# Performance work log

Hardware: AMD Instinct MI355X
Metric: run time of the kernel (lower is better)

The kernel has to match this reference:

```python
import jax, jax.numpy as jnp
from jax import lax
import numpy as np

NSTART, NOPEN, NHID, NCLOSE, NLAYERS, KSZ, N = 40, 128, 256, 3, 40, 9, 1024
H_STEP = 0.1
PAD = (KSZ - 1) // 2  # 4 -> same-length conv
EPS = 1e-5


def conv1(x, K):
    # x: (1, Cin, N), K: (Cout, Cin, k); cross-correlation like torch F.conv1d
    return lax.conv_general_dilated(x, K, (1,), [(PAD, PAD)],
                                    dimension_numbers=('NCH', 'OIH', 'NCH'))


def conv1T(x, K):
    # torch F.conv_transpose1d(x, K, padding=PAD) == conv1d with swapped-channel,
    # flipped kernel and padding k-1-PAD (= PAD here since k=9, PAD=4)
    Kt = jnp.flip(jnp.swapaxes(K, 0, 1), -1)
    return lax.conv_general_dilated(x, Kt, (1,), [(PAD, PAD)],
                                    dimension_numbers=('NCH', 'OIH', 'NCH'))


def instance_norm(x):
    # x: (1, C, N); normalize per channel over spatial dim, biased var, no affine
    m = jnp.mean(x, axis=-1, keepdims=True)
    v = jnp.var(x, axis=-1, keepdims=True)
    return (x - m) * lax.rsqrt(v + EPS)


def get_graph_lap(Z):
    # Z: (C, N). Normalized Gaussian-affinity graph Laplacian.
    sq = jnp.sum(Z * Z, axis=0)  # (N,)
    D2 = jnp.maximum(sq[:, None] + sq[None, :] - 2.0 * (Z.T @ Z), 0.0)
    sigma = jnp.mean(D2) + 1e-12
    Wg = jnp.exp(-D2 / sigma)
    deg = jnp.sum(Wg, axis=1)
    Dh = lax.rsqrt(deg)
    L = Dh[:, None] * (jnp.diag(deg) - Wg) * Dh[None, :]
    return L, deg


def double_sym_layer(Z, Wi, Bi, L):
    # Z: (nopen, N), Wi: (2, nhid, nopen, 9), Bi: (2, nopen, 1), L: (N, N)
    A0 = instance_norm(conv1((Z + Bi[0])[None], Wi[0]))
    A1 = instance_norm((conv1((Z + Bi[1])[None], Wi[1])[0] @ L)[None])
    A0 = jax.nn.relu(A0)
    A1 = jax.nn.relu(A1)
    A0 = conv1T(A0, Wi[0])[0]
    A1 = conv1T(A1, Wi[1])[0] @ L.T
    return A0 + A1  # (nopen, N)


def setup_inputs() -> dict:
    key = jax.random.key(0)
    k1, k2, k3, k4, k5 = jax.random.split(key, 5)
    Z = jax.random.normal(k1, (NSTART, N), dtype=jnp.float32)
    stdv_o = 0.001 * NOPEN / NSTART
    Kopen = jax.random.uniform(k2, (NOPEN, NSTART), minval=-stdv_o, maxval=stdv_o, dtype=jnp.float32)
    stdv_c = 0.001 * NCLOSE / NOPEN
    Kclose = jax.random.uniform(k3, (NCLOSE, NOPEN), minval=-stdv_c, maxval=stdv_c, dtype=jnp.float32)
    W = jax.random.uniform(k4, (NLAYERS, 2, NHID, NOPEN, KSZ), minval=-1e-4, maxval=1e-4, dtype=jnp.float32)
    Bias = jax.random.uniform(k5, (NLAYERS, 2, NOPEN, 1), dtype=jnp.float32) * 1e-4
    return {"Z": Z, "Kopen": Kopen, "Kclose": Kclose, "W": W, "Bias": Bias}


def reference(Z, Kopen, Kclose, W, Bias):
    h = H_STEP
    Zc = Kopen @ Z          # (nopen, N)
    Zold = Zc
    L, _ = get_graph_lap(Zc)
    for i in range(NLAYERS):
        if i % 10 == 0:
            L, _ = get_graph_lap(Zc)
        Ai = double_sym_layer(Zc, W[i], Bias[i], L)
        Zc, Zold = 2.0 * Zc - Zold - (h * h) * Ai, Zc  # leapfrog step
    return (Kclose @ Zc, Kclose @ Zold)
```

## Files before the change

kernel.cpp:

```cpp
#include <hip/hip_runtime.h>

#define NN 1024
#define NOPEN 128
#define NHID 256
#define NSTART 40
#define NCLOSE 3
#define NLAYERS 40
#define KSZ 9

static constexpr float H2 = 0.01f;
static constexpr float IN_EPS = 1e-5f;

using floatx4 = __attribute__((ext_vector_type(4))) float;
using bfrag = __attribute__((ext_vector_type(8))) short;

__device__ __forceinline__ ushort f2bf(float f) {
    union { float f; unsigned u; } v; v.f = f;
    unsigned r = v.u + 0x7fffu + ((v.u >> 16) & 1u);
    return (ushort)(r >> 16);
}

__device__ __forceinline__ void prepw_piece(const float* __restrict__ W, ushort* __restrict__ Wf1,
                                            ushort* __restrict__ Wf2, int lb, int lsrc, int tid) {
    if (lb < 72) {
        int z = lb / 36, rem = lb % 36;
        int t = rem >> 2, q = rem & 3;
        const float* Wz = W + (size_t)(lsrc * 2 + z) * (NHID * NOPEN * KSZ);
        ushort* dst = Wf1 + (((size_t)(z * 9 + t) * 64 + q * 16) << 9);
#pragma unroll
        for (int r = 0; r < 32; ++r) {
            int ei = r * 256 + tid;
            int g = q * 4 + (ei >> 11);
            int kc = (ei >> 9) & 3;
            int lm = (ei >> 3) & 15, lq = (ei >> 7) & 3;
            int e = ei & 7;
            int co = g * 16 + lm, ci = kc * 32 + lq * 8 + e;
            dst[ei] = f2bf(Wz[co * (NOPEN * KSZ) + ci * KSZ + t]);
        }
    } else {
        int p2 = lb - 72;
        int z = p2 / 36, rem = p2 % 36;
        int t = rem >> 2, q = rem & 3;
        const float* Wz = W + (size_t)(lsrc * 2 + z) * (NHID * NOPEN * KSZ);
        ushort* dst = Wf2 + (((size_t)(z * 9 + t) * 64 + q * 16) << 9);
#pragma unroll
        for (int r = 0; r < 32; ++r) {
            int ei = r * 256 + tid;
            int fb = q * 16 + (ei >> 9);
            int g = fb >> 3, j = fb & 7;
            int lm = (ei >> 3) & 15, lq = (ei >> 7) & 3;
            int e = ei & 7;
            int ci = g * 16 + lm, co = j * 32 + lq * 8 + e;
            dst[ei] = f2bf(Wz[co * (NOPEN * KSZ) + ci * KSZ + t]);
        }
    }
}

__global__ __launch_bounds__(256) void k_open(const float* __restrict__ Kopen, const float* __restrict__ Z,
                       float* __restrict__ Zc, float* __restrict__ Zold,
                       const float* __restrict__ Bias0, ushort* __restrict__ Zct,
                       ushort* __restrict__ At0, ushort* __restrict__ At1,
                       const float* __restrict__ W, ushort* __restrict__ Wf1,
                       ushort* __restrict__ Wf2, float* __restrict__ sig, float* __restrict__ A1) {
    const int v = blockIdx.x, tid = threadIdx.x;
    if (v < 512) {
        int o = v >> 2, n = (v & 3) * 256 + tid;
        float acc = 0.f;
#pragma unroll
        for (int s = 0; s < NSTART; ++s)
            acc = fmaf(Kopen[o * NSTART + s], Z[s * NN + n], acc);
        Zc[o * NN + n] = acc;
        Zold[o * NN + n] = acc;
#pragma unroll
        for (int z = 0; z < 2; ++z)
            Zct[z * (1032 * 128) + (n + 4) * 128 + o] = f2bf(acc + Bias0[z * NOPEN + o]);
    } else if (v < 656) {
        prepw_piece(W, Wf1, Wf2, v - 512, 0, tid);
    } else if (v == 656) {
        if (tid == 0) sig[0] = 0.f;
        for (int idx = tid; idx < 1024; idx += 256) {
            int z = idx >> 9, rr = idx & 511;
            ushort* Zz = Zct + z * (1032 * 128);
            Zz[rr] = 0; Zz[1028 * 128 + rr] = 0;
        }
        for (int idx = tid; idx < 2048; idx += 256) {
            int a = idx >> 10, rr = idx & 1023;
            ushort* A = a ? At1 : At0;
            A[rr] = 0; A[1028 * 256 + rr] = 0;
        }
    } else {
        int b = v - 657;
        size_t base = (size_t)b * 4096 + tid * 4;
        float4 z4 = {0.f, 0.f, 0.f, 0.f};
#pragma unroll
        for (int r = 0; r < 4; ++r) *(float4*)&A1[base + r * 1024] = z4;
    }
}

__global__ __launch_bounds__(256) void k_d2(const float* __restrict__ Zc,
                                            float* __restrict__ D2, float* __restrict__ sig) {
    __shared__ __align__(16) float Zi[32 * 36];
    __shared__ __align__(16) float Zj[32 * 68];
    __shared__ float sqi[32], sqj[64];
    __shared__ float red[4];
    const int tid = threadIdx.x;
    const int tx = tid & 15, ty = tid >> 4;
    const int j0 = blockIdx.x * 64, i0 = blockIdx.y * 32;
    if (tid < 32) sqi[tid] = 0.f;
    else if (tid < 96) sqj[tid - 32] = 0.f;
    float acc[2][4] = {};
    for (int c0 = 0; c0 < NOPEN; c0 += 32) {
        for (int idx = tid; idx < 32 * 32; idx += 256) {
            int c = idx >> 5, ii = idx & 31;
            Zi[c * 36 + ii] = Zc[(c0 + c) * NN + i0 + ii];
        }
        for (int idx = tid; idx < 32 * 64; idx += 256) {
            int c = idx >> 6, jj = idx & 63;
            Zj[c * 68 + jj] = Zc[(c0 + c) * NN + j0 + jj];
        }
        __syncthreads();
        if (tid < 32) {
            float s = 0.f;
            for (int c = 0; c < 32; ++c) { float x = Zi[c * 36 + tid]; s = fmaf(x, x, s); }
            sqi[tid] += s;
        } else if (tid < 96) {
            int jj = tid - 32;
            float s = 0.f;
            for (int c = 0; c < 32; ++c) { float x = Zj[c * 68 + jj]; s = fmaf(x, x, s); }
            sqj[jj] += s;
        }
#pragma unroll 8
        for (int c = 0; c < 32; ++c) {
            float2 zi = *(const float2*)&Zi[c * 36 + ty * 2];
            float4 zj = *(const float4*)&Zj[c * 68 + tx * 4];
            acc[0][0] = fmaf(zi.x, zj.x, acc[0][0]);
            acc[0][1] = fmaf(zi.x, zj.y, acc[0][1]);
            acc[0][2] = fmaf(zi.x, zj.z, acc[0][2]);
            acc[0][3] = fmaf(zi.x, zj.w, acc[0][3]);
            acc[1][0] = fmaf(zi.y, zj.x, acc[1][0]);
            acc[1][1] = fmaf(zi.y, zj.y, acc[1][1]);
            acc[1][2] = fmaf(zi.y, zj.z, acc[1][2]);
            acc[1][3] = fmaf(zi.y, zj.w, acc[1][3]);
        }
        __syncthreads();
    }
    float part = 0.f;
#pragma unroll
    for (int m = 0; m < 2; ++m) {
        int i = i0 + ty * 2 + m;
        float sqi_v = sqi[ty * 2 + m];
        float4 d;
        d.x = fmaxf(sqi_v + sqj[tx * 4 + 0] - 2.f * acc[m][0], 0.f);
        d.y = fmaxf(sqi_v + sqj[tx * 4 + 1] - 2.f * acc[m][1], 0.f);
        d.z = fmaxf(sqi_v + sqj[tx * 4 + 2] - 2.f * acc[m][2], 0.f);
        d.w = fmaxf(sqi_v + sqj[tx * 4 + 3] - 2.f * acc[m][3], 0.f);
        *(float4*)&D2[(size_t)i * NN + j0 + tx * 4] = d;
        part += (d.x + d.y) + (d.z + d.w);
    }
#pragma unroll
    for (int off = 32; off > 0; off >>= 1) part += __shfl_down(part, off);
    if ((tid & 63) == 0) red[tid >> 6] = part;
    __syncthreads();
    if (tid == 0) atomicAdd(sig, red[0] + red[1] + red[2] + red[3]);
}

__global__ void k_deg(const float* __restrict__ D2, const float* __restrict__ sig,
                      float* __restrict__ Dh) {
    __shared__ float red[4];
    int i = blockIdx.x, tid = threadIdx.x;
    float inv = 1.f / (sig[0] * (1.f / 1048576.f) + 1e-12f);
    float4 v = *(const float4*)&D2[(size_t)i * NN + tid * 4];
    float s = __expf(-v.x * inv) + __expf(-v.y * inv) + __expf(-v.z * inv) + __expf(-v.w * inv);
#pragma unroll
    for (int off = 32; off > 0; off >>= 1) s += __shfl_down(s, off);
    if ((tid & 63) == 0) red[tid >> 6] = s;
    __syncthreads();
    if (tid == 0) Dh[i] = rsqrtf(red[0] + red[1] + red[2] + red[3]);
}

__global__ void k_L(const float* __restrict__ D2, const float* __restrict__ sig,
                    const float* __restrict__ Dh, ushort* __restrict__ Lb) {
    int i = blockIdx.x, tid = threadIdx.x;
    int j = tid * 4;
    float inv = 1.f / (sig[0] * (1.f / 1048576.f) + 1e-12f);
    float dhi = Dh[i];
    float4 v = *(const float4*)&D2[(size_t)i * NN + j];
    float4 dj = *(const float4*)&Dh[j];
    float4 o;
    o.x = -dhi * dj.x * __expf(-v.x * inv);
    o.y = -dhi * dj.y * __expf(-v.y * inv);
    o.z = -dhi * dj.z * __expf(-v.z * inv);
    o.w = -dhi * dj.w * __expf(-v.w * inv);
    if (i == j + 0) o.x += 1.f;
    if (i == j + 1) o.y += 1.f;
    if (i == j + 2) o.z += 1.f;
    if (i == j + 3) o.w += 1.f;
    ushort4 ob; ob.x = f2bf(o.x); ob.y = f2bf(o.y); ob.z = f2bf(o.z); ob.w = f2bf(o.w);
    *(ushort4*)&Lb[(size_t)i * NN + j] = ob;
}

__global__ __launch_bounds__(256) void k_conv(const ushort* __restrict__ Zct,
        const ushort* __restrict__ Wf1, float* __restrict__ C0, ushort* __restrict__ C1b) {
    const int z = blockIdx.z;
    const int p0 = blockIdx.x * 64, co0 = blockIdx.y * 32;
    __shared__ ushort Xs[72 * 136];
    const int tid = threadIdx.x;
    const ushort* Zz = Zct + z * (1032 * 128);
    for (int idx = tid; idx < 1152; idx += 256) {
        int row = idx >> 4, ch = (idx & 15) * 8;
        *(bfrag*)&Xs[row * 136 + ch] = *(const bfrag*)&Zz[(p0 + row) * 128 + ch];
    }
    __syncthreads();
    const int l = tid & 63, wv = tid >> 6;
    const int wm = wv >> 1, wn = wv & 1;
    const int lm = l & 15, lq = l >> 4;
    const ushort* wf = Wf1 + (((size_t)z * 144 + (blockIdx.y * 2 + wm)) << 11) + l * 8;
    floatx4 acc[2] = {};
    bfrag a_cur[4];
#pragma unroll
    for (int kc = 0; kc < 4; ++kc) a_cur[kc] = *(const bfrag*)(wf + (kc << 9));
    for (int t = 0; t < 9; ++t) {
        bfrag a_nxt[4];
        if (t < 8) {
            const ushort* wptr = wf + (size_t)(t + 1) * (16 << 11);
#pragma unroll
            for (int kc = 0; kc < 4; ++kc) a_nxt[kc] = *(const bfrag*)(wptr + (kc << 9));
        }
        const int xbase = (wn * 32 + lm + t) * 136 + lq * 8;
#pragma unroll
        for (int kc = 0; kc < 4; ++kc) {
            bfrag b0 = *(const bfrag*)&Xs[xbase + kc * 32];
            acc[0] = __builtin_amdgcn_mfma_f32_16x16x32_bf16(a_cur[kc], b0, acc[0], 0, 0, 0);
            bfrag b1 = *(const bfrag*)&Xs[xbase + 16 * 136 + kc * 32];
            acc[1] = __builtin_amdgcn_mfma_f32_16x16x32_bf16(a_cur[kc], b1, acc[1], 0, 0, 0);
        }
#pragma unroll
        for (int kc = 0; kc < 4; ++kc) a_cur[kc] = a_nxt[kc];
    }
    const int cog = co0 + wm * 16 + lq * 4;
    const int pg = p0 + wn * 32 + lm;
#pragma unroll
    for (int j = 0; j < 2; ++j)
#pragma unroll
        for (int r = 0; r < 4; ++r) {
            if (z == 0) C0[(cog + r) * NN + pg + j * 16] = acc[j][r];
            else        C1b[(cog + r) * NN + pg + j * 16] = f2bf(acc[j][r]);
        }
}

__global__ __launch_bounds__(256) void k_xl_mfma(const ushort* __restrict__ X,
                                                 const ushort* __restrict__ Lb,
                                                 float* __restrict__ Out) {
    __shared__ __align__(16) ushort As[64 * 136];
    __shared__ __align__(16) ushort Bs[128 * 136];
    const int tid = threadIdx.x;
    const int lane = tid & 63, wave = tid >> 6;
    const int wm = wave >> 1, wn = wave & 1;
    const int n0 = blockIdx.x * 128, m0 = blockIdx.y * 64, kc = blockIdx.z * 128;
    {
        int q = tid;
#pragma unroll
        for (int r = 0; r < 4; ++r, q += 256) {
            int row = q >> 4, ch = (q & 15) * 8;
            *(bfrag*)&As[row * 136 + ch] = *(const bfrag*)&X[(m0 + row) * NN + kc + ch];
        }
        q = tid;
#pragma unroll
        for (int r = 0; r < 8; ++r, q += 256) {
            int row = q >> 4, ch = (q & 15) * 8;
            *(bfrag*)&Bs[row * 136 + ch] = *(const bfrag*)&Lb[(n0 + row) * NN + kc + ch];
        }
    }
    __syncthreads();
    floatx4 acc[2][4] = {};
    const int lrow = (lane & 15) * 136;
    const int koff = (lane >> 4) * 8;
#pragma unroll
    for (int ks = 0; ks < 4; ++ks) {
        bfrag a[2], b[4];
#pragma unroll
        for (int i = 0; i < 2; ++i)
            a[i] = *(const bfrag*)&As[(wm * 32 + i * 16) * 136 + lrow + ks * 32 + koff];
#pragma unroll
        for (int j = 0; j < 4; ++j)
            b[j] = *(const bfrag*)&Bs[(wn * 64 + j * 16) * 136 + lrow + ks * 32 + koff];
#pragma unroll
        for (int i = 0; i < 2; ++i)
#pragma unroll
            for (int j = 0; j < 4; ++j)
                acc[i][j] = __builtin_amdgcn_mfma_f32_16x16x32_bf16(a[i], b[j], acc[i][j], 0, 0, 0);
    }
    const int mg0 = m0 + wm * 32 + (lane >> 4) * 4;
    const int ng0 = n0 + wn * 64 + (lane & 15);
#pragma unroll
    for (int i = 0; i < 2; ++i)
#pragma unroll
        for (int j = 0; j < 4; ++j)
#pragma unroll
            for (int r = 0; r < 4; ++r)
                atomicAdd(&Out[(size_t)(mg0 + i * 16 + r) * NN + ng0 + j * 16], acc[i][j][r]);
}

__global__ void k_inorm(const float* __restrict__ C0, const float* __restrict__ A1,
                        float* __restrict__ Mu, float* __restrict__ Rs) {
    const int c = blockIdx.x, arr = blockIdx.y, tid = threadIdx.x;
    __shared__ float rs[4], rq[4];
    const float* in = arr ? A1 : C0;
    float4 v = *(const float4*)&in[c * NN + tid * 4];
    float s = (v.x + v.y) + (v.z + v.w);
    float q = (v.x * v.x + v.y * v.y) + (v.z * v.z + v.w * v.w);
#pragma unroll
    for (int off = 32; off > 0; off >>= 1) { s += __shfl_down(s, off); q += __shfl_down(q, off); }
    if ((tid & 63) == 0) { rs[tid >> 6] = s; rq[tid >> 6] = q; }
    __syncthreads();
    if (tid == 0) {
        float S = rs[0] + rs[1] + rs[2] + rs[3];
        float Q = rq[0] + rq[1] + rq[2] + rq[3];
        float mean = S * (1.f / NN);
        float var = Q * (1.f / NN) - mean * mean;
        Mu[arr * NHID + c] = mean;
        Rs[arr * NHID + c] = rsqrtf(var + IN_EPS);
    }
}

__global__ __launch_bounds__(256) void k_normT(const float* __restrict__ C0,
        const float* __restrict__ A1, const float* __restrict__ Mu, const float* __restrict__ Rs,
        ushort* __restrict__ At0, ushort* __restrict__ At1) {
    const int arr = blockIdx.z;
    const int p0 = blockIdx.x * 64, co0 = blockIdx.y * 64;
    const float* in = arr ? A1 : C0;
    ushort* out = arr ? At1 : At0;
    __shared__ ushort Ls[64 * 72];
    const int tid = threadIdx.x;
#pragma unroll
    for (int r = 0; r < 4; ++r) {
        int idx = r * 256 + tid;
        int col = idx >> 4, pq = idx & 15;
        int co = co0 + col;
        float4 v = *(const float4*)&in[(size_t)co * NN + p0 + pq * 4];
        float m = Mu[arr * NHID + co], sc = Rs[arr * NHID + co];
        Ls[(pq * 4 + 0) * 72 + col] = f2bf(fmaxf((v.x - m) * sc, 0.f));
        Ls[(pq * 4 + 1) * 72 + col] = f2bf(fmaxf((v.y - m) * sc, 0.f));
        Ls[(pq * 4 + 2) * 72 + col] = f2bf(fmaxf((v.z - m) * sc, 0.f));
        Ls[(pq * 4 + 3) * 72 + col] = f2bf(fmaxf((v.w - m) * sc, 0.f));
    }
    __syncthreads();
#pragma unroll
    for (int r = 0; r < 2; ++r) {
        int idx = r * 256 + tid;
        int row = idx >> 3, ch = (idx & 7) * 8;
        *(bfrag*)&out[(size_t)(p0 + row + 4) * 256 + co0 + ch] = *(const bfrag*)&Ls[row * 72 + ch];
    }
}

__global__ __launch_bounds__(256) void k_convT(const ushort* __restrict__ At0,
        const ushort* __restrict__ At1, const ushort* __restrict__ Wf2,
        float* __restrict__ Tacc, ushort* __restrict__ T1b) {
    const int z = blockIdx.z;
    const int p0 = blockIdx.x * 64, ci0 = blockIdx.y * 16;
    __shared__ ushort Al[72 * 264];
    const ushort* A = z ? At1 : At0;
    const int tid = threadIdx.x;
    for (int idx = tid; idx < 2304; idx += 256) {
        int row = idx >> 5, ch = (idx & 31) * 8;
        *(bfrag*)&Al[row * 264 + ch] = *(const bfrag*)&A[(p0 + row) * 256 + ch];
    }
    __syncthreads();
    const int l = tid & 63, wv = tid >> 6;
    const int lm = l & 15, lq = l >> 4;
    const ushort* wf = Wf2 + (((size_t)z * 72 + blockIdx.y) << 12) + l * 8;
    floatx4 acc0 = {}, acc1 = {};
    bfrag a_cur[8];
#pragma unroll
    for (int j = 0; j < 8; ++j) a_cur[j] = *(const bfrag*)(wf + (j << 9));
    for (int t = 0; t < 9; ++t) {
        bfrag a_nxt[8];
        if (t < 8) {
            const ushort* wptr = wf + (size_t)(t + 1) * (8 << 12);
#pragma unroll
            for (int j = 0; j < 8; ++j) a_nxt[j] = *(const bfrag*)(wptr + (j << 9));
        }
        const int abase = (wv * 16 + lm + 8 - t) * 264 + lq * 8;
#pragma unroll
        for (int j = 0; j < 8; j += 2) {
            bfrag b0 = *(const bfrag*)&Al[abase + j * 32];
            acc0 = __builtin_amdgcn_mfma_f32_16x16x32_bf16(a_cur[j], b0, acc0, 0, 0, 0);
            bfrag b1 = *(const bfrag*)&Al[abase + j * 32 + 32];
            acc1 = __builtin_amdgcn_mfma_f32_16x16x32_bf16(a_cur[j + 1], b1, acc1, 0, 0, 0);
        }
#pragma unroll
        for (int j = 0; j < 8; ++j) a_cur[j] = a_nxt[j];
    }
    floatx4 acc = acc0 + acc1;
    const int cig = ci0 + lq * 4;
    const int pg = p0 + wv * 16 + lm;
#pragma unroll
    for (int r = 0; r < 4; ++r) {
        if (z == 0) Tacc[(cig + r) * NN + pg] = acc[r];
        else        T1b[(cig + r) * NN + pg] = f2bf(acc[r]);
    }
}

__global__ __launch_bounds__(256) void k_leap(const float* __restrict__ Tacc,
        const float* __restrict__ Zc, float* __restrict__ Zo,
        const float* __restrict__ BiasN, ushort* __restrict__ Zct,
        const float* __restrict__ W, ushort* __restrict__ Wf1, ushort* __restrict__ Wf2,
        float* __restrict__ A1, float* __restrict__ sig, int lnext, int doprep) {
    const int v = blockIdx.x, tid = threadIdx.x;
    if (v < 128) {
        int off = (v * 256 + tid) * 4;
        float4 a = *(const float4*)&Tacc[off];
        float4 zc = *(const float4*)&Zc[off];
        float4 zo = *(const float4*)&Zo[off];
        float4 zn;
        zn.x = 2.f * zc.x - zo.x - H2 * a.x;
        zn.y = 2.f * zc.y - zo.y - H2 * a.y;
        zn.z = 2.f * zc.z - zo.z - H2 * a.z;
        zn.w = 2.f * zc.w - zo.w - H2 * a.w;
        *(float4*)&Zo[off] = zn;
        int ci = off >> 10, n = off & 1023;
#pragma unroll
        for (int z = 0; z < 2; ++z) {
            float bz = BiasN[z * NOPEN + ci];
            ushort* Zz = Zct + z * (1032 * 128);
            Zz[(n + 4) * 128 + ci] = f2bf(zn.x + bz);
            Zz[(n + 5) * 128 + ci] = f2bf(zn.y + bz);
            Zz[(n + 6) * 128 + ci] = f2bf(zn.z + bz);
            Zz[(n + 7) * 128 + ci] = f2bf(zn.w + bz);
        }
    } else if (v < 272) {
        if (doprep) prepw_piece(W, Wf1, Wf2, v - 128, lnext, tid);
    } else if (v == 272) {
        if (tid == 0) sig[0] = 0.f;
    } else {
        int b = v - 273;
        size_t base = (size_t)b * 4096 + tid * 4;
        float4 z4 = {0.f, 0.f, 0.f, 0.f};
#pragma unroll
        for (int r = 0; r < 4; ++r) *(float4*)&A1[base + r * 1024] = z4;
    }
}

__global__ void k_close(const float* __restrict__ Kclose, const float* __restrict__ Zc,
                        const float* __restrict__ Zold, float* __restrict__ out) {
    int n = blockIdx.x * 256 + threadIdx.x;
    int o = blockIdx.y;
    const float* Zb = blockIdx.z ? Zold : Zc;
    float a = 0.f;
#pragma unroll
    for (int c = 0; c < NOPEN; ++c) a = fmaf(Kclose[o * NOPEN + c], Zb[c * NN + n], a);
    out[blockIdx.z * (NCLOSE * NN) + o * NN + n] = a;
}

extern "C" void kernel_launch(void* const* d_in, const int* in_sizes, int n_in,
                              void* d_out, int out_size, void* d_ws, size_t ws_size,
                              hipStream_t stream) {
    const float* Z      = (const float*)d_in[0];
    const float* Kopen  = (const float*)d_in[1];
    const float* Kclose = (const float*)d_in[2];
    const float* W      = (const float*)d_in[3];
    const float* Bias   = (const float*)d_in[4];
    float* out = (float*)d_out;
    float* ws  = (float*)d_ws;

    float* Zb0   = ws + 0;
    float* Zb1   = ws + 131072;
    float* D2    = ws + 262144;
    float* C0    = ws + 1310720;
    float* A1    = ws + 1572864;
    float* Tacc  = ws + 1835008;
    float* Dh    = ws + 5111808;
    float* sig   = ws + 5112832;
    float* Mu    = ws + 5113856;
    float* Rs    = ws + 5114880;
    ushort* Lb  = (ushort*)(ws + 5115904);
    ushort* C1b = (ushort*)(ws + 5640192);
    ushort* T1b = (ushort*)(ws + 5771264);
    ushort* Zct = (ushort*)(ws + 5836800);
    ushort* At0 = (ushort*)(ws + 5968896);
    ushort* At1 = (ushort*)(ws + 6100992);
    ushort* Wf1 = (ushort*)(ws + 6233088);
    ushort* Wf2 = (ushort*)(ws + 6528000);

    k_open<<<dim3(721), 256, 0, stream>>>(Kopen, Z, Zb0, Zb1, Bias, Zct, At0, At1,
                                          W, Wf1, Wf2, sig, A1);

    float* Zc = Zb0;
    float* Zold = Zb1;
    for (int i = 0; i < NLAYERS; ++i) {
        if (i % 10 == 0) {
            k_d2<<<dim3(16, 32), 256, 0, stream>>>(Zc, D2, sig);
            k_deg<<<dim3(NN), 256, 0, stream>>>(D2, sig, Dh);
            k_L<<<dim3(NN), 256, 0, stream>>>(D2, sig, Dh, Lb);
        }
        k_conv<<<dim3(16, 8, 2), 256, 0, stream>>>(Zct, Wf1, C0, C1b);
        k_xl_mfma<<<dim3(8, 4, 8), 256, 0, stream>>>(C1b, Lb, A1);
        k_inorm<<<dim3(NHID, 2), 256, 0, stream>>>(C0, A1, Mu, Rs);
        k_normT<<<dim3(16, 4, 2), 256, 0, stream>>>(C0, A1, Mu, Rs, At0, At1);
        k_convT<<<dim3(16, 8, 2), 256, 0, stream>>>(At0, At1, Wf2, Tacc, T1b);
        k_xl_mfma<<<dim3(8, 2, 8), 256, 0, stream>>>(T1b, Lb, Tacc);
        int lnext = (i + 1 < NLAYERS) ? i + 1 : NLAYERS - 1;
        k_leap<<<dim3(337), 256, 0, stream>>>(Tacc, Zc, Zold,
                                              Bias + (size_t)lnext * 2 * NOPEN, Zct,
                                              W, Wf1, Wf2, A1, sig, lnext, (i + 1 < NLAYERS) ? 1 : 0);
        float* tmp = Zc; Zc = Zold; Zold = tmp;
    }

    k_close<<<dim3(4, NCLOSE, 2), 256, 0, stream>>>(Kclose, Zc, Zold, out);
}
```

Before: 2.092 ms.

## Fuse per-layer pipeline: stats in GEMM epilogues, norm into convT, L-GEMM into leapfrog

Cuts the per-layer chain from six kernels to four. Instance-norm statistics are now gathered with shuffles and atomics in the conv and first L-GEMM epilogues, replacing the separate k_inorm pass. The normalize and transpose step is folded into the transposed-conv kernel's shared-memory load, and the second L-GEMM is fused with the leapfrog update. The split-K atomic GEMMs become full-K loops, so A1 and Tacc no longer need zeroing. The cost is fewer blocks per launch (64, 64 and 128), which lowers parallelism, and the single-pass variance formula is less numerically robust.

```diff
diff --git a/kernel.cpp b/kernel.cpp
--- a/kernel.cpp
+++ b/kernel.cpp
@@ -59,9 +59,8 @@
 __global__ __launch_bounds__(256) void k_open(const float* __restrict__ Kopen, const float* __restrict__ Z,
                        float* __restrict__ Zc, float* __restrict__ Zold,
                        const float* __restrict__ Bias0, ushort* __restrict__ Zct,
-                       ushort* __restrict__ At0, ushort* __restrict__ At1,
                        const float* __restrict__ W, ushort* __restrict__ Wf1,
-                       ushort* __restrict__ Wf2, float* __restrict__ sig, float* __restrict__ A1) {
+                       ushort* __restrict__ Wf2, float* __restrict__ sig, float* __restrict__ Stats) {
     const int v = blockIdx.x, tid = threadIdx.x;
     if (v < 512) {
         int o = v >> 2, n = (v & 3) * 256 + tid;
@@ -76,24 +75,14 @@
             Zct[z * (1032 * 128) + (n + 4) * 128 + o] = f2bf(acc + Bias0[z * NOPEN + o]);
     } else if (v < 656) {
         prepw_piece(W, Wf1, Wf2, v - 512, 0, tid);
-    } else if (v == 656) {
+    } else {
         if (tid == 0) sig[0] = 0.f;
+        for (int idx = tid; idx < 1024; idx += 256) Stats[idx] = 0.f;
         for (int idx = tid; idx < 1024; idx += 256) {
             int z = idx >> 9, rr = idx & 511;
             ushort* Zz = Zct + z * (1032 * 128);
             Zz[rr] = 0; Zz[1028 * 128 + rr] = 0;
         }
-        for (int idx = tid; idx < 2048; idx += 256) {
-            int a = idx >> 10, rr = idx & 1023;
-            ushort* A = a ? At1 : At0;
-            A[rr] = 0; A[1028 * 256 + rr] = 0;
-        }
-    } else {
-        int b = v - 657;
-        size_t base = (size_t)b * 4096 + tid * 4;
-        float4 z4 = {0.f, 0.f, 0.f, 0.f};
-#pragma unroll
-        for (int r = 0; r < 4; ++r) *(float4*)&A1[base + r * 1024] = z4;
     }
 }
 
@@ -200,7 +189,8 @@
 }
 
 __global__ __launch_bounds__(256) void k_conv(const ushort* __restrict__ Zct,
-        const ushort* __restrict__ Wf1, float* __restrict__ C0, ushort* __restrict__ C1b) {
+        const ushort* __restrict__ Wf1, float* __restrict__ C0, ushort* __restrict__ C1b,
+        float* __restrict__ Stats) {
     const int z = blockIdx.z;
     const int p0 = blockIdx.x * 64, co0 = blockIdx.y * 32;
     __shared__ ushort Xs[72 * 136];
@@ -246,198 +236,226 @@
             if (z == 0) C0[(cog + r) * NN + pg + j * 16] = acc[j][r];
             else        C1b[(cog + r) * NN + pg + j * 16] = f2bf(acc[j][r]);
         }
-}
-
-__global__ __launch_bounds__(256) void k_xl_mfma(const ushort* __restrict__ X,
-                                                 const ushort* __restrict__ Lb,
-                                                 float* __restrict__ Out) {
-    __shared__ __align__(16) ushort As[64 * 136];
+    if (z == 0) {
+        float s[4], q2[4];
+#pragma unroll
+        for (int r = 0; r < 4; ++r) {
+            s[r] = acc[0][r] + acc[1][r];
+            q2[r] = acc[0][r] * acc[0][r] + acc[1][r] * acc[1][r];
+        }
+#pragma unroll
+        for (int off = 1; off < 16; off <<= 1)
+#pragma unroll
+            for (int r = 0; r < 4; ++r) {
+                s[r] += __shfl_xor(s[r], off);
+                q2[r] += __shfl_xor(q2[r], off);
+            }
+        if (lm == 0)
+#pragma unroll
+            for (int r = 0; r < 4; ++r) {
+                atomicAdd(&Stats[cog + r], s[r]);
+                atomicAdd(&Stats[256 + cog + r], q2[r]);
+            }
+    }
+}
+
+__global__ __launch_bounds__(256) void k_xl1(const ushort* __restrict__ X,
+                                             const ushort* __restrict__ Lb,
+                                             float* __restrict__ A1, float* __restrict__ Stats) {
+    __shared__ __align__(16) ushort As[32 * 136];
     __shared__ __align__(16) ushort Bs[128 * 136];
     const int tid = threadIdx.x;
     const int lane = tid & 63, wave = tid >> 6;
     const int wm = wave >> 1, wn = wave & 1;
-    const int n0 = blockIdx.x * 128, m0 = blockIdx.y * 64, kc = blockIdx.z * 128;
+    const int lm = lane & 15, lq = lane >> 4;
+    const int n0 = blockIdx.x * 128, m0 = blockIdx.y * 32;
+    floatx4 acc[4] = {};
+    for (int kc = 0; kc < 1024; kc += 128) {
+        __syncthreads();
+        {
+            int q = tid;
+#pragma unroll
+            for (int r = 0; r < 2; ++r, q += 256) {
+                int row = q >> 4, ch = (q & 15) * 8;
+                *(bfrag*)&As[row * 136 + ch] = *(const bfrag*)&X[(m0 + row) * NN + kc + ch];
+            }
+            q = tid;
+#pragma unroll
+            for (int r = 0; r < 8; ++r, q += 256) {
+                int row = q >> 4, ch = (q & 15) * 8;
+                *(bfrag*)&Bs[row * 136 + ch] = *(const bfrag*)&Lb[(n0 + row) * NN + kc + ch];
+            }
+        }
+        __syncthreads();
+#pragma unroll
+        for (int ks = 0; ks < 4; ++ks) {
+            bfrag a = *(const bfrag*)&As[(wm * 16 + lm) * 136 + ks * 32 + lq * 8];
+#pragma unroll
+            for (int j = 0; j < 4; ++j) {
+                bfrag b = *(const bfrag*)&Bs[(wn * 64 + j * 16 + lm) * 136 + ks * 32 + lq * 8];
+                acc[j] = __builtin_amdgcn_mfma_f32_16x16x32_bf16(a, b, acc[j], 0, 0, 0);
+            }
+        }
+    }
+    const int mg0 = m0 + wm * 16 + lq * 4;
+    const int ng0 = n0 + wn * 64 + lm;
+#pragma unroll
+    for (int j = 0; j < 4; ++j)
+#pragma unroll
+        for (int r = 0; r < 4; ++r)
+            A1[(size_t)(mg0 + r) * NN + ng0 + j * 16] = acc[j][r];
+    float s[4], q2[4];
+#pragma unroll
+    for (int r = 0; r < 4; ++r) {
+        s[r] = (acc[0][r] + acc[1][r]) + (acc[2][r] + acc[3][r]);
+        q2[r] = (acc[0][r] * acc[0][r] + acc[1][r] * acc[1][r]) +
+                (acc[2][r] * acc[2][r] + acc[3][r] * acc[3][r]);
+    }
+#pragma unroll
+    for (int off = 1; off < 16; off <<= 1)
+#pragma unroll
+        for (int r = 0; r < 4; ++r) {
+            s[r] += __shfl_xor(s[r], off);
+            q2[r] += __shfl_xor(q2[r], off);
+        }
+    if (lm == 0)
+#pragma unroll
+        for (int r = 0; r < 4; ++r) {
+            atomicAdd(&Stats[512 + mg0 + r], s[r]);
+            atomicAdd(&Stats[768 + mg0 + r], q2[r]);
+        }
+}
+
+__global__ __launch_bounds__(256) void k_nct(const float* __restrict__ C0, const float* __restrict__ A1,
+        const float* __restrict__ Stats, const ushort* __restrict__ Wf2,
+        float* __restrict__ Tacc, ushort* __restrict__ T1b) {
+    const int z = blockIdx.z;
+    const int cih = blockIdx.y;
+    const int p0 = blockIdx.x * 64;
+    __shared__ ushort Al[72 * 264];
+    const int tid = threadIdx.x;
+    const float* in = z ? A1 : C0;
     {
-        int q = tid;
-#pragma unroll
-        for (int r = 0; r < 4; ++r, q += 256) {
-            int row = q >> 4, ch = (q & 15) * 8;
-            *(bfrag*)&As[row * 136 + ch] = *(const bfrag*)&X[(m0 + row) * NN + kc + ch];
-        }
-        q = tid;
-#pragma unroll
-        for (int r = 0; r < 8; ++r, q += 256) {
-            int row = q >> 4, ch = (q & 15) * 8;
-            *(bfrag*)&Bs[row * 136 + ch] = *(const bfrag*)&Lb[(n0 + row) * NN + kc + ch];
-        }
-    }
-    __syncthreads();
-    floatx4 acc[2][4] = {};
-    const int lrow = (lane & 15) * 136;
-    const int koff = (lane >> 4) * 8;
-#pragma unroll
-    for (int ks = 0; ks < 4; ++ks) {
-        bfrag a[2], b[4];
-#pragma unroll
-        for (int i = 0; i < 2; ++i)
-            a[i] = *(const bfrag*)&As[(wm * 32 + i * 16) * 136 + lrow + ks * 32 + koff];
-#pragma unroll
-        for (int j = 0; j < 4; ++j)
-            b[j] = *(const bfrag*)&Bs[(wn * 64 + j * 16) * 136 + lrow + ks * 32 + koff];
-#pragma unroll
-        for (int i = 0; i < 2; ++i)
-#pragma unroll
-            for (int j = 0; j < 4; ++j)
-                acc[i][j] = __builtin_amdgcn_mfma_f32_16x16x32_bf16(a[i], b[j], acc[i][j], 0, 0, 0);
-    }
-    const int mg0 = m0 + wm * 32 + (lane >> 4) * 4;
-    const int ng0 = n0 + wn * 64 + (lane & 15);
-#pragma unroll
-    for (int i = 0; i < 2; ++i)
-#pragma unroll
-        for (int j = 0; j < 4; ++j)
-#pragma unroll
-            for (int r = 0; r < 4; ++r)
-                atomicAdd(&Out[(size_t)(mg0 + i * 16 + r) * NN + ng0 + j * 16], acc[i][j][r]);
-}
-
-__global__ void k_inorm(const float* __restrict__ C0, const float* __restrict__ A1,
-                        float* __restrict__ Mu, float* __restrict__ Rs) {
-    const int c = blockIdx.x, arr = blockIdx.y, tid = threadIdx.x;
-    __shared__ float rs[4], rq[4];
-    const float* in = arr ? A1 : C0;
-    float4 v = *(const float4*)&in[c * NN + tid * 4];
-    float s = (v.x + v.y) + (v.z + v.w);
-    float q = (v.x * v.x + v.y * v.y) + (v.z * v.z + v.w * v.w);
-#pragma unroll
-    for (int off = 32; off > 0; off >>= 1) { s += __shfl_down(s, off); q += __shfl_down(q, off); }
-    if ((tid & 63) == 0) { rs[tid >> 6] = s; rq[tid >> 6] = q; }
-    __syncthreads();
-    if (tid == 0) {
-        float S = rs[0] + rs[1] + rs[2] + rs[3];
-        float Q = rq[0] + rq[1] + rq[2] + rq[3];
+        const int co = tid;
+        float S = Stats[z * 512 + co], Q = Stats[z * 512 + 256 + co];
         float mean = S * (1.f / NN);
         float var = Q * (1.f / NN) - mean * mean;
-        Mu[arr * NHID + c] = mean;
-        Rs[arr * NHID + c] = rsqrtf(var + IN_EPS);
-    }
-}
-
-__global__ __launch_bounds__(256) void k_normT(const float* __restrict__ C0,
-        const float* __restrict__ A1, const float* __restrict__ Mu, const float* __restrict__ Rs,
-        ushort* __restrict__ At0, ushort* __restrict__ At1) {
-    const int arr = blockIdx.z;
-    const int p0 = blockIdx.x * 64, co0 = blockIdx.y * 64;
-    const float* in = arr ? A1 : C0;
-    ushort* out = arr ? At1 : At0;
-    __shared__ ushort Ls[64 * 72];
-    const int tid = threadIdx.x;
-#pragma unroll
-    for (int r = 0; r < 4; ++r) {
-        int idx = r * 256 + tid;
-        int col = idx >> 4, pq = idx & 15;
-        int co = co0 + col;
-        float4 v = *(const float4*)&in[(size_t)co * NN + p0 + pq * 4];
-        float m = Mu[arr * NHID + co], sc = Rs[arr * NHID + co];
-        Ls[(pq * 4 + 0) * 72 + col] = f2bf(fmaxf((v.x - m) * sc, 0.f));
-        Ls[(pq * 4 + 1) * 72 + col] = f2bf(fmaxf((v.y - m) * sc, 0.f));
-        Ls[(pq * 4 + 2) * 72 + col] = f2bf(fmaxf((v.z - m) * sc, 0.f));
-        Ls[(pq * 4 + 3) * 72 + col] = f2bf(fmaxf((v.w - m) * sc, 0.f));
-    }
-    __syncthreads();
-#pragma unroll
-    for (int r = 0; r < 2; ++r) {
-        int idx = r * 256 + tid;
-        int row = idx >> 3, ch = (idx & 7) * 8;
-        *(bfrag*)&out[(size_t)(p0 + row + 4) * 256 + co0 + ch] = *(const bfrag*)&Ls[row * 72 + ch];
-    }
-}
-
-__global__ __launch_bounds__(256) void k_convT(const ushort* __restrict__ At0,
-        const ushort* __restrict__ At1, const ushort* __restrict__ Wf2,
-        float* __restrict__ Tacc, ushort* __restrict__ T1b) {
-    const int z = blockIdx.z;
-    const int p0 = blockIdx.x * 64, ci0 = blockIdx.y * 16;
-    __shared__ ushort Al[72 * 264];
-    const ushort* A = z ? At1 : At0;
-    const int tid = threadIdx.x;
-    for (int idx = tid; idx < 2304; idx += 256) {
-        int row = idx >> 5, ch = (idx & 31) * 8;
-        *(bfrag*)&Al[row * 264 + ch] = *(const bfrag*)&A[(p0 + row) * 256 + ch];
+        float rs = rsqrtf(var + IN_EPS);
+        const float* row = in + (size_t)co * NN;
+#pragma unroll
+        for (int k = 0; k < 18; ++k) {
+            int p = p0 - 4 + k * 4;
+            float4 v;
+            if ((unsigned)p < 1024u) v = *(const float4*)&row[p];
+            else { v.x = v.y = v.z = v.w = 0.f; }
+            Al[(k * 4 + 0) * 264 + co] = f2bf(fmaxf((v.x - mean) * rs, 0.f));
+            Al[(k * 4 + 1) * 264 + co] = f2bf(fmaxf((v.y - mean) * rs, 0.f));
+            Al[(k * 4 + 2) * 264 + co] = f2bf(fmaxf((v.z - mean) * rs, 0.f));
+            Al[(k * 4 + 3) * 264 + co] = f2bf(fmaxf((v.w - mean) * rs, 0.f));
+        }
     }
     __syncthreads();
     const int l = tid & 63, wv = tid >> 6;
     const int lm = l & 15, lq = l >> 4;
-    const ushort* wf = Wf2 + (((size_t)z * 72 + blockIdx.y) << 12) + l * 8;
-    floatx4 acc0 = {}, acc1 = {};
-    bfrag a_cur[8];
-#pragma unroll
-    for (int j = 0; j < 8; ++j) a_cur[j] = *(const bfrag*)(wf + (j << 9));
+    floatx4 acc[4] = {};
+    const ushort* wz = Wf2 + (((size_t)z * 72 + cih * 4) << 12) + l * 8;
     for (int t = 0; t < 9; ++t) {
-        bfrag a_nxt[8];
-        if (t < 8) {
-            const ushort* wptr = wf + (size_t)(t + 1) * (8 << 12);
-#pragma unroll
-            for (int j = 0; j < 8; ++j) a_nxt[j] = *(const bfrag*)(wptr + (j << 9));
-        }
         const int abase = (wv * 16 + lm + 8 - t) * 264 + lq * 8;
-#pragma unroll
-        for (int j = 0; j < 8; j += 2) {
-            bfrag b0 = *(const bfrag*)&Al[abase + j * 32];
-            acc0 = __builtin_amdgcn_mfma_f32_16x16x32_bf16(a_cur[j], b0, acc0, 0, 0, 0);
-            bfrag b1 = *(const bfrag*)&Al[abase + j * 32 + 32];
-            acc1 = __builtin_amdgcn_mfma_f32_16x16x32_bf16(a_cur[j + 1], b1, acc1, 0, 0, 0);
-        }
-#pragma unroll
-        for (int j = 0; j < 8; ++j) a_cur[j] = a_nxt[j];
-    }
-    floatx4 acc = acc0 + acc1;
-    const int cig = ci0 + lq * 4;
+        const ushort* wt = wz + (size_t)t * (8 << 12);
+#pragma unroll
+        for (int j = 0; j < 8; ++j) {
+            bfrag b = *(const bfrag*)&Al[abase + j * 32];
+#pragma unroll
+            for (int sub = 0; sub < 4; ++sub) {
+                bfrag a = *(const bfrag*)(wt + ((size_t)sub << 12) + (j << 9));
+                acc[sub] = __builtin_amdgcn_mfma_f32_16x16x32_bf16(a, b, acc[sub], 0, 0, 0);
+            }
+        }
+    }
     const int pg = p0 + wv * 16 + lm;
 #pragma unroll
-    for (int r = 0; r < 4; ++r) {
-        if (z == 0) Tacc[(cig + r) * NN + pg] = acc[r];
-        else        T1b[(cig + r) * NN + pg] = f2bf(acc[r]);
-    }
-}
-
-__global__ __launch_bounds__(256) void k_leap(const float* __restrict__ Tacc,
+    for (int sub = 0; sub < 4; ++sub) {
+        int cig = cih * 64 + sub * 16 + lq * 4;
+#pragma unroll
+        for (int r = 0; r < 4; ++r) {
+            if (z == 0) Tacc[(cig + r) * NN + pg] = acc[sub][r];
+            else        T1b[(cig + r) * NN + pg] = f2bf(acc[sub][r]);
+        }
+    }
+}
+
+__global__ __launch_bounds__(256) void k_xl2leap(const ushort* __restrict__ T1b,
+        const ushort* __restrict__ Lb, const float* __restrict__ Tacc,
         const float* __restrict__ Zc, float* __restrict__ Zo,
         const float* __restrict__ BiasN, ushort* __restrict__ Zct,
         const float* __restrict__ W, ushort* __restrict__ Wf1, ushort* __restrict__ Wf2,
-        float* __restrict__ A1, float* __restrict__ sig, int lnext, int doprep) {
-    const int v = blockIdx.x, tid = threadIdx.x;
-    if (v < 128) {
-        int off = (v * 256 + tid) * 4;
-        float4 a = *(const float4*)&Tacc[off];
-        float4 zc = *(const float4*)&Zc[off];
-        float4 zo = *(const float4*)&Zo[off];
-        float4 zn;
-        zn.x = 2.f * zc.x - zo.x - H2 * a.x;
-        zn.y = 2.f * zc.y - zo.y - H2 * a.y;
-        zn.z = 2.f * zc.z - zo.z - H2 * a.z;
-        zn.w = 2.f * zc.w - zo.w - H2 * a.w;
-        *(float4*)&Zo[off] = zn;
-        int ci = off >> 10, n = off & 1023;
-#pragma unroll
-        for (int z = 0; z < 2; ++z) {
-            float bz = BiasN[z * NOPEN + ci];
-            ushort* Zz = Zct + z * (1032 * 128);
-            Zz[(n + 4) * 128 + ci] = f2bf(zn.x + bz);
-            Zz[(n + 5) * 128 + ci] = f2bf(zn.y + bz);
-            Zz[(n + 6) * 128 + ci] = f2bf(zn.z + bz);
-            Zz[(n + 7) * 128 + ci] = f2bf(zn.w + bz);
-        }
-    } else if (v < 272) {
-        if (doprep) prepw_piece(W, Wf1, Wf2, v - 128, lnext, tid);
-    } else if (v == 272) {
-        if (tid == 0) sig[0] = 0.f;
-    } else {
-        int b = v - 273;
-        size_t base = (size_t)b * 4096 + tid * 4;
-        float4 z4 = {0.f, 0.f, 0.f, 0.f};
-#pragma unroll
-        for (int r = 0; r < 4; ++r) *(float4*)&A1[base + r * 1024] = z4;
+        float* __restrict__ Stats, float* __restrict__ sig, int lnext, int doprep) {
+    const int b = blockIdx.x, tid = threadIdx.x;
+    __shared__ __align__(16) ushort As[16 * 136];
+    __shared__ __align__(16) ushort Bs[64 * 136];
+    __shared__ __align__(16) ushort Zt[2 * 64 * 16];
+    if (b >= 128) {
+        if (b < 272) {
+            if (doprep) prepw_piece(W, Wf1, Wf2, b - 128, lnext, tid);
+        } else {
+            if (tid == 0) sig[0] = 0.f;
+            float4 z4 = {0.f, 0.f, 0.f, 0.f};
+            *(float4*)&Stats[tid * 4] = z4;
+        }
+        return;
+    }
+    const int nt = b >> 3, mt = b & 7;
+    const int n0 = nt * 64, m0 = mt * 16;
+    const int lane = tid & 63, wv = tid >> 6;
+    const int lm = lane & 15, lq = lane >> 4;
+    floatx4 acc = {};
+    for (int kc = 0; kc < 1024; kc += 128) {
+        __syncthreads();
+        {
+            int row = tid >> 4, ch = (tid & 15) * 8;
+            *(bfrag*)&As[row * 136 + ch] = *(const bfrag*)&T1b[(m0 + row) * NN + kc + ch];
+#pragma unroll
+            for (int r = 0; r < 4; ++r) {
+                int q = r * 256 + tid;
+                int row2 = q >> 4, ch2 = (q & 15) * 8;
+                *(bfrag*)&Bs[row2 * 136 + ch2] = *(const bfrag*)&Lb[(n0 + row2) * NN + kc + ch2];
+            }
+        }
+        __syncthreads();
+#pragma unroll
+        for (int ks = 0; ks < 4; ++ks) {
+            bfrag a = *(const bfrag*)&As[lm * 136 + ks * 32 + lq * 8];
+            bfrag bb = *(const bfrag*)&Bs[(wv * 16 + lm) * 136 + ks * 32 + lq * 8];
+            acc = __builtin_amdgcn_mfma_f32_16x16x32_bf16(a, bb, acc, 0, 0, 0);
+        }
+    }
+    const int n = n0 + wv * 16 + lm;
+    float zn[4];
+#pragma unroll
+    for (int r = 0; r < 4; ++r) {
+        int m = m0 + lq * 4 + r;
+        float a = acc[r] + Tacc[(size_t)m * NN + n];
+        float zc = Zc[(size_t)m * NN + n];
+        float zo = Zo[(size_t)m * NN + n];
+        zn[r] = 2.f * zc - zo - H2 * a;
+        Zo[(size_t)m * NN + n] = zn[r];
+    }
+#pragma unroll
+    for (int z = 0; z < 2; ++z)
+#pragma unroll
+        for (int r = 0; r < 4; ++r) {
+            int ml = lq * 4 + r;
+            float bz = BiasN[z * NOPEN + m0 + ml];
+            Zt[z * 1024 + (wv * 16 + lm) * 16 + ml] = f2bf(zn[r] + bz);
+        }
+    __syncthreads();
+    if (tid < 128) {
+        int zz = tid >> 6, nl = tid & 63;
+        bfrag v0 = *(const bfrag*)&Zt[zz * 1024 + nl * 16];
+        bfrag v1 = *(const bfrag*)&Zt[zz * 1024 + nl * 16 + 8];
+        ushort* dst = Zct + zz * (1032 * 128) + (size_t)(n0 + nl + 4) * 128 + m0;
+        *(bfrag*)&dst[0] = v0;
+        *(bfrag*)&dst[8] = v1;
     }
 }
 
@@ -469,21 +487,18 @@
     float* C0    = ws + 1310720;
     float* A1    = ws + 1572864;
     float* Tacc  = ws + 1835008;
+    float* Stats = ws + 1966080;
     float* Dh    = ws + 5111808;
     float* sig   = ws + 5112832;
-    float* Mu    = ws + 5113856;
-    float* Rs    = ws + 5114880;
     ushort* Lb  = (ushort*)(ws + 5115904);
     ushort* C1b = (ushort*)(ws + 5640192);
     ushort* T1b = (ushort*)(ws + 5771264);
     ushort* Zct = (ushort*)(ws + 5836800);
-    ushort* At0 = (ushort*)(ws + 5968896);
-    ushort* At1 = (ushort*)(ws + 6100992);
     ushort* Wf1 = (ushort*)(ws + 6233088);
     ushort* Wf2 = (ushort*)(ws + 6528000);
 
-    k_open<<<dim3(721), 256, 0, stream>>>(Kopen, Z, Zb0, Zb1, Bias, Zct, At0, At1,
-                                          W, Wf1, Wf2, sig, A1);
+    k_open<<<dim3(657), 256, 0, stream>>>(Kopen, Z, Zb0, Zb1, Bias, Zct,
+                                          W, Wf1, Wf2, sig, Stats);
 
     float* Zc = Zb0;
     float* Zold = Zb1;
@@ -493,16 +508,14 @@
             k_deg<<<dim3(NN), 256, 0, stream>>>(D2, sig, Dh);
             k_L<<<dim3(NN), 256, 0, stream>>>(D2, sig, Dh, Lb);
         }
-        k_conv<<<dim3(16, 8, 2), 256, 0, stream>>>(Zct, Wf1, C0, C1b);
-        k_xl_mfma<<<dim3(8, 4, 8), 256, 0, stream>>>(C1b, Lb, A1);
-        k_inorm<<<dim3(NHID, 2), 256, 0, stream>>>(C0, A1, Mu, Rs);
-        k_normT<<<dim3(16, 4, 2), 256, 0, stream>>>(C0, A1, Mu, Rs, At0, At1);
-        k_convT<<<dim3(16, 8, 2), 256, 0, stream>>>(At0, At1, Wf2, Tacc, T1b);
-        k_xl_mfma<<<dim3(8, 2, 8), 256, 0, stream>>>(T1b, Lb, Tacc);
+        k_conv<<<dim3(16, 8, 2), 256, 0, stream>>>(Zct, Wf1, C0, C1b, Stats);
+        k_xl1<<<dim3(8, 8), 256, 0, stream>>>(C1b, Lb, A1, Stats);
+        k_nct<<<dim3(16, 2, 2), 256, 0, stream>>>(C0, A1, Stats, Wf2, Tacc, T1b);
         int lnext = (i + 1 < NLAYERS) ? i + 1 : NLAYERS - 1;
-        k_leap<<<dim3(337), 256, 0, stream>>>(Tacc, Zc, Zold,
-                                              Bias + (size_t)lnext * 2 * NOPEN, Zct,
-                                              W, Wf1, Wf2, A1, sig, lnext, (i + 1 < NLAYERS) ? 1 : 0);
+        k_xl2leap<<<dim3(273), 256, 0, stream>>>(T1b, Lb, Tacc, Zc, Zold,
+                                                 Bias + (size_t)lnext * 2 * NOPEN, Zct,
+                                                 W, Wf1, Wf2, Stats, sig, lnext,
+                                                 (i + 1 < NLAYERS) ? 1 : 0);
         float* tmp = Zc; Zc = Zold; Zold = tmp;
     }
 
```

Result: slower. 3.318 ms (+58.6%).

## Fuse instance-norm statistics into conv epilogue and normT, drop k_inorm

Applied to the files above, without the earlier changes.

Removes the separate k_inorm launch per layer. For the plain conv branch, per-channel sum and sum-of-squares are reduced inside k_conv's epilogue via wave shuffles and atomics into a Stats buffer, zeroed in k_leap/k_open. For the Laplacian branch, each k_normT block recomputes its 64 channels' statistics by scanning full rows, trading redundant L2 reads and atomics for one fewer kernel launch and sync point.

```diff
diff --git a/kernel.cpp b/kernel.cpp
--- a/kernel.cpp
+++ b/kernel.cpp
@@ -61,7 +61,8 @@
                        const float* __restrict__ Bias0, ushort* __restrict__ Zct,
                        ushort* __restrict__ At0, ushort* __restrict__ At1,
                        const float* __restrict__ W, ushort* __restrict__ Wf1,
-                       ushort* __restrict__ Wf2, float* __restrict__ sig, float* __restrict__ A1) {
+                       ushort* __restrict__ Wf2, float* __restrict__ sig,
+                       float* __restrict__ A1, float* __restrict__ Stats) {
     const int v = blockIdx.x, tid = threadIdx.x;
     if (v < 512) {
         int o = v >> 2, n = (v & 3) * 256 + tid;
@@ -78,6 +79,7 @@
         prepw_piece(W, Wf1, Wf2, v - 512, 0, tid);
     } else if (v == 656) {
         if (tid == 0) sig[0] = 0.f;
+        for (int idx = tid; idx < 512; idx += 256) Stats[idx] = 0.f;
         for (int idx = tid; idx < 1024; idx += 256) {
             int z = idx >> 9, rr = idx & 511;
             ushort* Zz = Zct + z * (1032 * 128);
@@ -200,7 +202,8 @@
 }
 
 __global__ __launch_bounds__(256) void k_conv(const ushort* __restrict__ Zct,
-        const ushort* __restrict__ Wf1, float* __restrict__ C0, ushort* __restrict__ C1b) {
+        const ushort* __restrict__ Wf1, float* __restrict__ C0, ushort* __restrict__ C1b,
+        float* __restrict__ Stats) {
     const int z = blockIdx.z;
     const int p0 = blockIdx.x * 64, co0 = blockIdx.y * 32;
     __shared__ ushort Xs[72 * 136];
@@ -246,6 +249,27 @@
             if (z == 0) C0[(cog + r) * NN + pg + j * 16] = acc[j][r];
             else        C1b[(cog + r) * NN + pg + j * 16] = f2bf(acc[j][r]);
         }
+    if (z == 0) {
+        float s[4], q2[4];
+#pragma unroll
+        for (int r = 0; r < 4; ++r) {
+            s[r] = acc[0][r] + acc[1][r];
+            q2[r] = acc[0][r] * acc[0][r] + acc[1][r] * acc[1][r];
+        }
+#pragma unroll
+        for (int off = 1; off < 16; off <<= 1)
+#pragma unroll
+            for (int r = 0; r < 4; ++r) {
+                s[r] += __shfl_xor(s[r], off);
+                q2[r] += __shfl_xor(q2[r], off);
+            }
+        if (lm == 0)
+#pragma unroll
+            for (int r = 0; r < 4; ++r) {
+                atomicAdd(&Stats[cog + r], s[r]);
+                atomicAdd(&Stats[256 + cog + r], q2[r]);
+            }
+    }
 }
 
 __global__ __launch_bounds__(256) void k_xl_mfma(const ushort* __restrict__ X,
@@ -301,44 +325,54 @@
                 atomicAdd(&Out[(size_t)(mg0 + i * 16 + r) * NN + ng0 + j * 16], acc[i][j][r]);
 }
 
-__global__ void k_inorm(const float* __restrict__ C0, const float* __restrict__ A1,
-                        float* __restrict__ Mu, float* __restrict__ Rs) {
-    const int c = blockIdx.x, arr = blockIdx.y, tid = threadIdx.x;
-    __shared__ float rs[4], rq[4];
-    const float* in = arr ? A1 : C0;
-    float4 v = *(const float4*)&in[c * NN + tid * 4];
-    float s = (v.x + v.y) + (v.z + v.w);
-    float q = (v.x * v.x + v.y * v.y) + (v.z * v.z + v.w * v.w);
-#pragma unroll
-    for (int off = 32; off > 0; off >>= 1) { s += __shfl_down(s, off); q += __shfl_down(q, off); }
-    if ((tid & 63) == 0) { rs[tid >> 6] = s; rq[tid >> 6] = q; }
-    __syncthreads();
-    if (tid == 0) {
-        float S = rs[0] + rs[1] + rs[2] + rs[3];
-        float Q = rq[0] + rq[1] + rq[2] + rq[3];
-        float mean = S * (1.f / NN);
-        float var = Q * (1.f / NN) - mean * mean;
-        Mu[arr * NHID + c] = mean;
-        Rs[arr * NHID + c] = rsqrtf(var + IN_EPS);
-    }
-}
-
 __global__ __launch_bounds__(256) void k_normT(const float* __restrict__ C0,
-        const float* __restrict__ A1, const float* __restrict__ Mu, const float* __restrict__ Rs,
+        const float* __restrict__ A1, const float* __restrict__ Stats,
         ushort* __restrict__ At0, ushort* __restrict__ At1) {
     const int arr = blockIdx.z;
     const int p0 = blockIdx.x * 64, co0 = blockIdx.y * 64;
     const float* in = arr ? A1 : C0;
     ushort* out = arr ? At1 : At0;
     __shared__ ushort Ls[64 * 72];
+    __shared__ float mu[64], rs[64];
+    __shared__ float pS[256], pQ[256];
     const int tid = threadIdx.x;
+    if (arr == 0) {
+        if (tid < 64) {
+            int co = co0 + tid;
+            float S = Stats[co], Q = Stats[256 + co];
+            float mean = S * (1.f / NN);
+            float var = Q * (1.f / NN) - mean * mean;
+            mu[tid] = mean;
+            rs[tid] = rsqrtf(var + IN_EPS);
+        }
+    } else {
+        int ch = tid >> 2, sub = tid & 3;
+        const float* row = in + (size_t)(co0 + ch) * NN;
+        float s = 0.f, qq = 0.f;
+        for (int k = 0; k < 64; ++k) {
+            float4 v = *(const float4*)&row[k * 16 + sub * 4];
+            s += (v.x + v.y) + (v.z + v.w);
+            qq += (v.x * v.x + v.y * v.y) + (v.z * v.z + v.w * v.w);
+        }
+        pS[tid] = s; pQ[tid] = qq;
+        __syncthreads();
+        if (tid < 64) {
+            int base = tid * 4;
+            float S = (pS[base] + pS[base + 1]) + (pS[base + 2] + pS[base + 3]);
+            float Q = (pQ[base] + pQ[base + 1]) + (pQ[base + 2] + pQ[base + 3]);
+            float mean = S * (1.f / NN);
+            float var = Q * (1.f / NN) - mean * mean;
+            mu[tid] = mean;
+            rs[tid] = rsqrtf(var + IN_EPS);
+        }
+    }
+    __syncthreads();
 #pragma unroll
     for (int r = 0; r < 4; ++r) {
         int idx = r * 256 + tid;
         int col = idx >> 4, pq = idx & 15;
-        int co = co0 + col;
-        float4 v = *(const float4*)&in[(size_t)co * NN + p0 + pq * 4];
-        float m = Mu[arr * NHID + co], sc = Rs[arr * NHID + co];
+        float4 v = *(const float4*)&in[(size_t)(co0 + col) * NN + p0 + pq * 4];
+        float m = mu[col], sc = rs[col];
         Ls[(pq * 4 + 0) * 72 + col] = f2bf(fmaxf((v.x - m) * sc, 0.f));
         Ls[(pq * 4 + 1) * 72 + col] = f2bf(fmaxf((v.y - m) * sc, 0.f));
         Ls[(pq * 4 + 2) * 72 + col] = f2bf(fmaxf((v.z - m) * sc, 0.f));
@@ -405,7 +439,8 @@
         const float* __restrict__ Zc, float* __restrict__ Zo,
         const float* __restrict__ BiasN, ushort* __restrict__ Zct,
         const float* __restrict__ W, ushort* __restrict__ Wf1, ushort* __restrict__ Wf2,
-        float* __restrict__ A1, float* __restrict__ sig, int lnext, int doprep) {
+        float* __restrict__ A1, float* __restrict__ Stats, float* __restrict__ sig,
+        int lnext, int doprep) {
     const int v = blockIdx.x, tid = threadIdx.x;
     if (v < 128) {
         int off = (v * 256 + tid) * 4;
@@ -432,6 +467,10 @@
         if (doprep) prepw_piece(W, Wf1, Wf2, v - 128, lnext, tid);
     } else if (v == 272) {
         if (tid == 0) sig[0] = 0.f;
+        if (tid < 128) {
+            float4 z4 = {0.f, 0.f, 0.f, 0.f};
+            *(float4*)&Stats[tid * 4] = z4;
+        }
     } else {
         int b = v - 273;
         size_t base = (size_t)b * 4096 + tid * 4;
@@ -471,8 +510,7 @@
     float* Tacc  = ws + 1835008;
     float* Dh    = ws + 5111808;
     float* sig   = ws + 5112832;
-    float* Mu    = ws + 5113856;
-    float* Rs    = ws + 5114880;
+    float* Stats = ws + 5113856;
     ushort* Lb  = (ushort*)(ws + 5115904);
     ushort* C1b = (ushort*)(ws + 5640192);
     ushort* T1b = (ushort*)(ws + 5771264);
@@ -483,7 +521,7 @@
     ushort* Wf2 = (ushort*)(ws + 6528000);
 
     k_open<<<dim3(721), 256, 0, stream>>>(Kopen, Z, Zb0, Zb1, Bias, Zct, At0, At1,
-                                          W, Wf1, Wf2, sig, A1);
+                                          W, Wf1, Wf2, sig, A1, Stats);
 
     float* Zc = Zb0;
     float* Zold = Zb1;
@@ -493,16 +531,16 @@
             k_deg<<<dim3(NN), 256, 0, stream>>>(D2, sig, Dh);
             k_L<<<dim3(NN), 256, 0, stream>>>(D2, sig, Dh, Lb);
         }
-        k_conv<<<dim3(16, 8, 2), 256, 0, stream>>>(Zct, Wf1, C0, C1b);
+        k_conv<<<dim3(16, 8, 2), 256, 0, stream>>>(Zct, Wf1, C0, C1b, Stats);
         k_xl_mfma<<<dim3(8, 4, 8), 256, 0, stream>>>(C1b, Lb, A1);
-        k_inorm<<<dim3(NHID, 2), 256, 0, stream>>>(C0, A1, Mu, Rs);
-        k_normT<<<dim3(16, 4, 2), 256, 0, stream>>>(C0, A1, Mu, Rs, At0, At1);
+        k_normT<<<dim3(16, 4, 2), 256, 0, stream>>>(C0, A1, Stats, At0, At1);
         k_convT<<<dim3(16, 8, 2), 256, 0, stream>>>(At0, At1, Wf2, Tacc, T1b);
         k_xl_mfma<<<dim3(8, 2, 8), 256, 0, stream>>>(T1b, Lb, Tacc);
         int lnext = (i + 1 < NLAYERS) ? i + 1 : NLAYERS - 1;
         k_leap<<<dim3(337), 256, 0, stream>>>(Tacc, Zc, Zold,
                                               Bias + (size_t)lnext * 2 * NOPEN, Zct,
-                                              W, Wf1, Wf2, A1, sig, lnext, (i + 1 < NLAYERS) ? 1 : 0);
+                                              W, Wf1, Wf2, A1, Stats, sig, lnext,
+                                              (i + 1 < NLAYERS) ? 1 : 0);
         float* tmp = Zc; Zc = Zold; Zold = tmp;
     }
 
```

New measurement: 2.249 ms. 7.5% more time.
